# Optimization experiments

Hardware: AMD Instinct MI355X
Metric: run time of the kernel (lower is better)

Reference implementation:

```python
import jax, jax.numpy as jnp
import numpy as np

B, T, D, E = 8, 2048, 256, 4
D_E = D // E


def setup_inputs() -> dict:
    key = jax.random.key(0)
    ks = jax.random.split(key, 12)
    s = 1.0 / np.sqrt(D)
    x = jax.random.normal(ks[0], (B, T, D), dtype=jnp.float32)
    # ensure max(seq_len) == T so the padded input matches this_batch_padlen
    seq_len = jnp.concatenate([
        jax.random.randint(ks[1], (B - 1,), T // 2, T),
        jnp.array([T]),
    ]).astype(jnp.int32)
    return {
        "x": x,
        "seq_len": seq_len,
        "wq": jax.random.uniform(ks[2], (D, D), jnp.float32, -s, s),
        "bq": jax.random.uniform(ks[3], (D,), jnp.float32, -s, s),
        "wk": jax.random.uniform(ks[4], (D, D), jnp.float32, -s, s),
        "bk": jax.random.uniform(ks[5], (D,), jnp.float32, -s, s),
        "wv": jax.random.uniform(ks[6], (D, D), jnp.float32, -s, s),
        "bv": jax.random.uniform(ks[7], (D,), jnp.float32, -s, s),
        "wo": jax.random.uniform(ks[8], (D, D), jnp.float32, -s, s),
        "bo": jax.random.uniform(ks[9], (D,), jnp.float32, -s, s),
        "theta": jnp.array([50.0], dtype=jnp.float32),
    }


def _split_heads(y):
    # faithful to torch: [B,T,D] -> permute(0,2,1) -> [B,D,T] -> reshape(B*E, T, D_E)
    return jnp.transpose(y, (0, 2, 1)).reshape(B * E, T, D_E)


def reference(x, seq_len, wq, bq, wk, bk, wv, bv, wo, bo, theta):
    Q = _split_heads(x @ wq.T + bq)          # [B*E, T, D_E]
    K = _split_heads(x @ wk.T + bk)          # [B*E, T, D_E]
    V = _split_heads(x @ wv.T + bv)          # [B*E, T, D_E]

    # padding mask: zero out query rows (and key cols) past seq_len[i]
    pos = jnp.arange(T)
    valid = (pos[None, :] < seq_len[:, None])                 # [B, T]
    mask_q = jnp.repeat(valid, E, axis=0).astype(Q.dtype)     # [B*E, T]
    Q = Q * mask_q[:, :, None]
    K = K * mask_q[:, :, None]

    scale = jnp.sqrt(jnp.float32(T))
    att = jnp.einsum('bqd,bkd->bqk', Q, K) / scale            # [B*E, T, T]

    # Gaussian positional penalty (is_punish=True)
    tpos = jnp.arange(T, dtype=jnp.float32)
    diff = tpos[None, :] - tpos[:, None]                      # j - i
    punish = jnp.exp(-(diff ** 2) / (theta[0] ** 2))          # [T, T]
    att = att * punish[None, :, :]

    att = jnp.where(att == 0.0, jnp.float32(-2e20), att)
    att = jax.nn.softmax(att, axis=2)

    ctx = jnp.einsum('bqk,bkd->bqd', att, V)                  # [B*E, T, D_E]
    # faithful inverse of _split_heads: permute(0,2,1)->reshape(B,D,T)->permute
    ctx = jnp.transpose(jnp.transpose(ctx, (0, 2, 1)).reshape(B, D, T), (0, 2, 1))
    A = ctx @ wo.T + bo
    return A + x
```

## Files before the change

### kernel.cpp

```cpp
#include <hip/hip_runtime.h>
#include <hip/hip_bf16.h>
#include <math.h>
#include <stdint.h>

#define B_SZ   8
#define T_SEQ  2048
#define DIM    256
#define NH     32
#define DE     64
#define BAND   509
#define M_ROWS (B_SZ * T_SEQ)

typedef __attribute__((ext_vector_type(8))) short short8;
typedef __attribute__((ext_vector_type(4))) float floatx4;
typedef __attribute__((ext_vector_type(4))) unsigned uintx4;
typedef unsigned short ushort_t;

__device__ __forceinline__ ushort_t f2bf(float x) {
    unsigned u = __float_as_uint(x);
    u += 0x7fffu + ((u >> 16) & 1u);
    return (ushort_t)(u >> 16);
}
__device__ __forceinline__ float bf2f(ushort_t b) {
    return __uint_as_float(((unsigned)b) << 16);
}
__device__ __forceinline__ unsigned pack2(float a, float b) {
    unsigned lo = __bfloat16_as_ushort(__float2bfloat16(a));
    unsigned hi = __bfloat16_as_ushort(__float2bfloat16(b));
    return lo | (hi << 16);
}

__device__ __forceinline__ double pd_exact(int d, float th) {
    float df  = (float)d;
    float arg = (-(df * df)) / (th * th);
    double pdd = exp((double)arg);
    if (pdd < 1.17549435082228751e-38)
        return rint(pdd * 0x1p149) * 0x1p-149;
    return (double)(float)pdd;
}

__global__ __launch_bounds__(256) void prep_kernel(
    const float* __restrict__ x,
    const float* __restrict__ wq, const float* __restrict__ wk,
    const float* __restrict__ wv, const float* __restrict__ wo,
    const float* __restrict__ theta,
    ushort_t* __restrict__ xb, ushort_t* __restrict__ wb,
    float* __restrict__ thr_g, float* __restrict__ pdf_g)
{
    const int bid = blockIdx.x, tid = threadIdx.x;
    if (bid < 2048) {
        size_t i8 = ((size_t)bid * 256 + tid) * 8;
        float4 a = *(const float4*)(x + i8);
        float4 b = *(const float4*)(x + i8 + 4);
        uint4 o;
        o.x = pack2(a.x, a.y); o.y = pack2(a.z, a.w);
        o.z = pack2(b.x, b.y); o.w = pack2(b.z, b.w);
        *(uint4*)(xb + i8) = o;
    } else if (bid < 2176) {
        size_t w8 = ((size_t)(bid - 2048) * 256 + tid) * 8;
        int which = (int)(w8 >> 16);
        const float* src = (which == 0) ? wq : (which == 1) ? wk : (which == 2) ? wv : wo;
        size_t off = w8 & 65535;
        float4 a = *(const float4*)(src + off);
        float4 b = *(const float4*)(src + off + 4);
        uint4 o;
        o.x = pack2(a.x, a.y); o.y = pack2(a.z, a.w);
        o.z = pack2(b.x, b.y); o.w = pack2(b.z, b.w);
        *(uint4*)(wb + w8) = o;
    } else {
        int i = (bid - 2176) * 256 + tid;
        float th = theta[0];
        if (i < 1024) {
            int d = i - 512;
            pdf_g[i] = (float)pd_exact(d, th) * 1.44269504088896340736f;
        }
        if (i < 1536) {
            int d = i - 768;
            int ad = d < 0 ? -d : d;
            if (ad < 321) {
                thr_g[i] = __builtin_inff();
            } else {
                double pdv = pd_exact(ad, th);
                thr_g[i] = (pdv == 0.0) ? __builtin_inff() : (float)(0x1p-150 / pdv);
            }
        }
    }
}

__global__ __launch_bounds__(256, 2) void proj_qkv_mfma(
    const ushort_t* __restrict__ xb, const ushort_t* __restrict__ wb,
    const float* __restrict__ bq, const float* __restrict__ bk,
    const float* __restrict__ bv, const int* __restrict__ seq_len,
    ushort_t* __restrict__ Qh, ushort_t* __restrict__ Kh, ushort_t* __restrict__ Vh)
{
    __shared__ __align__(16) ushort_t As[64][264];
    __shared__ __align__(16) ushort_t Ls[4][64][68];
    const int tid = threadIdx.x;
    const int wave = tid >> 6, lane = tid & 63;
    const int quad = lane >> 4, l15 = lane & 15;
    const int task = blockIdx.x * 4 + wave;
    const int nt64 = task % 12;
    const int mstrip = task / 12;
    const int mode = nt64 >> 2;
    const int nloc_base = (nt64 & 3) * 64;
    const ushort_t* Wp = wb + (size_t)mode * 65536;
    const int m0 = mstrip * 64;
    const int bb = m0 >> 11;
    const int th0 = (m0 >> 6) & 31;
    const int sl = seq_len[bb];
    ushort_t* outp = (mode == 0) ? Qh : (mode == 1) ? Kh : Vh;
    const float* bias = (mode == 0) ? bq : (mode == 1) ? bk : bv;
    const int hh = bb * 4 + (nloc_base >> 6);
    const float oscale = (mode == 0) ? 0.022097086912079612f : 1.0f;

    #pragma unroll
    for (int rep = 0; rep < 8; ++rep) {
        int f = rep * 256 + tid;
        int row = f >> 5, c8 = (f & 31) * 8;
        *(uint4*)&As[row][c8] = *(const uint4*)(xb + (size_t)(m0 + row) * 256 + c8);
    }

    short8 Bf[4][8];
    #pragma unroll
    for (int nt = 0; nt < 4; ++nt) {
        int nrow = nloc_base + nt * 16 + l15;
        #pragma unroll
        for (int ks = 0; ks < 8; ++ks)
            Bf[nt][ks] = *(const short8*)(Wp + (size_t)nrow * 256 + ks * 32 + quad * 8);
    }
    float bias4[4];
    #pragma unroll
    for (int nt = 0; nt < 4; ++nt) bias4[nt] = bias[nloc_base + nt * 16 + l15];

    __syncthreads();

    #pragma unroll
    for (int mb = 0; mb < 4; ++mb) {
        short8 Af[8];
        #pragma unroll
        for (int ks = 0; ks < 8; ++ks)
            Af[ks] = *(const short8*)&As[mb * 16 + l15][ks * 32 + quad * 8];
        floatx4 acc[4];
        #pragma unroll
        for (int nt = 0; nt < 4; ++nt) acc[nt] = (floatx4){0.f, 0.f, 0.f, 0.f};
        #pragma unroll
        for (int ks = 0; ks < 8; ++ks)
            #pragma unroll
            for (int nt = 0; nt < 4; ++nt)
                acc[nt] = __builtin_amdgcn_mfma_f32_16x16x32_bf16(Af[ks], Bf[nt][ks], acc[nt], 0, 0, 0);
        #pragma unroll
        for (int nt = 0; nt < 4; ++nt) {
            float v0 = (acc[nt][0] + bias4[nt]) * oscale;
            float v1 = (acc[nt][1] + bias4[nt]) * oscale;
            float v2 = (acc[nt][2] + bias4[nt]) * oscale;
            float v3 = (acc[nt][3] + bias4[nt]) * oscale;
            uint2 pk; pk.x = pack2(v0, v1); pk.y = pack2(v2, v3);
            *(uint2*)&Ls[wave][nt * 16 + l15][mb * 16 + quad * 4] = pk;
        }
    }

    #pragma unroll
    for (int s = 0; s < 16; ++s) {
        int dl = s * 4 + quad;
        int e0 = l15 * 4;
        uint2 pk = *(const uint2*)&Ls[wave][dl][e0];
        int q = dl * 32 + th0;
        if (mode <= 1 && q >= sl) { pk.x = 0u; pk.y = 0u; }
        *(uint2*)(outp + (((size_t)hh * T_SEQ + q) << 6) + e0) = pk;
    }
}

__global__ __launch_bounds__(256) void vtrans_kernel(const ushort_t* __restrict__ Vh,
                                                     ushort_t* __restrict__ VTp,
                                                     float* __restrict__ mv)
{
    __shared__ ushort_t Vs[256][66];
    __shared__ float red[32][72];
    const int tid = threadIdx.x;
    const int h = blockIdx.x >> 3, chunk = blockIdx.x & 7;
    const ushort_t* src = Vh + ((size_t)(h * T_SEQ + chunk * 256)) * DE;
    float s[8] = {};
    #pragma unroll
    for (int rep = 0; rep < 8; ++rep) {
        int f = rep * 256 + tid;
        int row = f >> 3, c8 = (f & 7) * 8;
        uint4 u = *(const uint4*)(src + (size_t)row * DE + c8);
        *(uint4*)&Vs[row][c8] = u;
        const ushort_t* w = (const ushort_t*)&u;
        #pragma unroll
        for (int i = 0; i < 8; ++i) s[i] += bf2f(w[i]);
    }
    {
        const int r0 = tid >> 3, es = (tid & 7) * 8;
        #pragma unroll
        for (int i = 0; i < 8; ++i) red[r0][es + i] = s[i];
    }
    __syncthreads();
    if (tid < 64) {
        float t = 0.f;
        #pragma unroll
        for (int g = 0; g < 32; ++g) t += red[g][tid];
        atomicAdd(&mv[h * DE + tid], t);
    }
    const int w = tid >> 6, lane = tid & 63;
    const int half = lane >> 5;
    const int c32 = lane & 31;
    const int cbase = c32 * 8;
    const int blk = cbase >> 6;
    const int cin = cbase & 63;
    #pragma unroll
    for (int rr = 0; rr < 8; ++rr) {
        int e = w * 16 + rr * 2 + half;
        ushort_t tmp[8];
        #pragma unroll
        for (int t = 0; t < 8; ++t) {
            int ci = cin + t;
            int j = blk * 64 + 32 * (ci >> 5) + 4 * ((ci >> 3) & 3)
                  + 16 * ((ci >> 2) & 1) + (ci & 3);
            tmp[t] = Vs[j][e];
        }
        *(uint4*)(VTp + ((size_t)(h * DE + e)) * T_SEQ + chunk * 256 + cbase) = *(uint4*)tmp;
    }
}

__global__ __launch_bounds__(512) void attn_mfma_kernel(
    const ushort_t* __restrict__ Qh, const ushort_t* __restrict__ Kh,
    const ushort_t* __restrict__ VTp, const float* __restrict__ thr_g,
    const float* __restrict__ pdf_g, const float* __restrict__ mvs,
    const int* __restrict__ seq_len, ushort_t* __restrict__ ctxb)
{
    __shared__ ushort_t Ks [2][64][72];
    __shared__ ushort_t VTs[2][64][72];
    __shared__ float pdfl[1024];
    __shared__ float thrc[1536];

    const int tid  = threadIdx.x;
    const int wave = tid >> 6;
    const int lane = tid & 63;
    const int quad = lane >> 4;
    const int l15  = lane & 15;
    const int bid   = blockIdx.x;
    const int inner = bid >> 3;
    const int g     = inner >> 4;
    const int strip = ((inner & 15) + g * 4) & 15;
    const int h  = (g << 3) | (bid & 7);
    const int q0 = strip * 128;
    const int b  = h >> 2;
    const int sl = seq_len[b];
    const float invT = 1.0f / (float)T_SEQ;
    ushort_t* outbase = ctxb + ((size_t)b * T_SEQ + q0) * DIM + (size_t)(h & 3) * 64;

    if (q0 >= sl) {
        #pragma unroll
        for (int nt = 0; nt < 4; ++nt) {
            ushort_t mval = f2bf(mvs[h * DE + l15 + 16 * nt] * invT);
            #pragma unroll
            for (int r = 0; r < 4; ++r)
                outbase[(size_t)(wave * 16 + quad * 4 + r) * DIM + l15 + 16 * nt] = mval;
        }
        return;
    }

    for (int i = tid; i < 1024; i += 512) pdfl[i] = pdf_g[i];
    for (int i = tid; i < 1536; i += 512) thrc[i] = thr_g[i];

    short8 qa0, qa1;
    {
        const ushort_t* qp = Qh + ((size_t)h * T_SEQ + q0 + wave * 16 + l15) * DE + quad * 8;
        qa0 = *(const short8*)(qp);
        qa1 = *(const short8*)(qp + 32);
    }

    float l_acc = 0.f;
    floatx4 cacc[4];
    #pragma unroll
    for (int nt = 0; nt < 4; ++nt) cacc[nt] = (floatx4){0.f, 0.f, 0.f, 0.f};

    int jlo = q0 - BAND;       if (jlo < 0) jlo = 0;
    int jhi = q0 + 127 + BAND; if (jhi > sl - 1) jhi = sl - 1;
    const int jt0 = jlo >> 6, jt1 = jhi >> 6;

    const int krow = tid >> 3;
    const int kc8  = (tid & 7) * 8;
    const ushort_t* Kbp = Kh + (size_t)h * T_SEQ * DE;
    const ushort_t* Vbp = VTp + (size_t)h * DE * T_SEQ;
    uint4 kpre0, kpre1, vpre0, vpre1;
    {
        const int ja = jt0 << 6;
        const int jb = ((jt0 + 1 <= jt1) ? jt0 + 1 : jt1) << 6;
        kpre0 = *(const uint4*)(Kbp + (size_t)(ja + krow) * DE + kc8);
        vpre0 = *(const uint4*)(Vbp + (size_t)krow * T_SEQ + ja + kc8);
        kpre1 = *(const uint4*)(Kbp + (size_t)(jb + krow) * DE + kc8);
        vpre1 = *(const uint4*)(Vbp + (size_t)krow * T_SEQ + jb + kc8);
    }

    const int qrow = q0 + wave * 16 + l15;

    auto subtile = [&](int s, int j0s) {
        floatx4 ST[4];
        #pragma unroll
        for (int nt = 0; nt < 4; ++nt) {
            short8 ka0 = *(const short8*)&Ks[s][l15 + 16 * nt][quad * 8];
            short8 ka1 = *(const short8*)&Ks[s][l15 + 16 * nt][32 + quad * 8];
            floatx4 z = {0.f, 0.f, 0.f, 0.f};
            z = __builtin_amdgcn_mfma_f32_16x16x32_bf16(ka0, qa0, z, 0, 0, 0);
            z = __builtin_amdgcn_mfma_f32_16x16x32_bf16(ka1, qa1, z, 0, 0, 0);
            ST[nt] = z;
        }

        const int offw = j0s - q0 - wave * 16;
        const int db   = j0s + quad * 4 - qrow;
        float p[4][4];
        if (offw > -384 && offw < 336) {
            if (j0s + 63 < sl) {
                #pragma unroll
                for (int nt = 0; nt < 4; ++nt)
                    #pragma unroll
                    for (int r = 0; r < 4; ++r)
                        p[nt][r] = __builtin_amdgcn_exp2f(
                            ST[nt][r] * pdfl[db + 512 + nt * 16 + r]);
            } else {
                #pragma unroll
                for (int nt = 0; nt < 4; ++nt)
                    #pragma unroll
                    for (int r = 0; r < 4; ++r) {
                        float v = __builtin_amdgcn_exp2f(
                            ST[nt][r] * pdfl[db + 512 + nt * 16 + r]);
                        p[nt][r] = (j0s + nt * 16 + quad * 4 + r < sl) ? v : 0.f;
                    }
            }
        } else {
            #pragma unroll
            for (int nt = 0; nt < 4; ++nt)
                #pragma unroll
                for (int r = 0; r < 4; ++r)
                    p[nt][r] = (fabsf(ST[nt][r]) > thrc[db + 768 + nt * 16 + r])
                               ? 1.0f : 0.0f;
        }

        #pragma unroll
        for (int nt = 0; nt < 4; ++nt)
            l_acc += (p[nt][0] + p[nt][1]) + (p[nt][2] + p[nt][3]);

        uintx4 t0, t1;
        t0.x = pack2(p[0][0], p[0][1]); t0.y = pack2(p[0][2], p[0][3]);
        t0.z = pack2(p[1][0], p[1][1]); t0.w = pack2(p[1][2], p[1][3]);
        t1.x = pack2(p[2][0], p[2][1]); t1.y = pack2(p[2][2], p[2][3]);
        t1.z = pack2(p[3][0], p[3][1]); t1.w = pack2(p[3][2], p[3][3]);
        short8 pa0 = __builtin_bit_cast(short8, t0);
        short8 pa1 = __builtin_bit_cast(short8, t1);

        #pragma unroll
        for (int nt = 0; nt < 4; ++nt) {
            short8 vb0 = *(const short8*)&VTs[s][l15 + 16 * nt][quad * 8];
            short8 vb1 = *(const short8*)&VTs[s][l15 + 16 * nt][32 + quad * 8];
            floatx4 c = cacc[nt];
            c = __builtin_amdgcn_mfma_f32_16x16x32_bf16(pa0, vb0, c, 0, 0, 0);
            c = __builtin_amdgcn_mfma_f32_16x16x32_bf16(pa1, vb1, c, 0, 0, 0);
            cacc[nt] = c;
        }
    };

    for (int jt = jt0; jt <= jt1; jt += 2) {
        const int j0a = jt << 6;
        const bool has_b = (jt + 1 <= jt1);
        const int j0b = (has_b ? jt + 1 : jt1) << 6;
        __syncthreads();
        *(uint4*)&Ks [0][krow][kc8] = kpre0;
        *(uint4*)&VTs[0][krow][kc8] = vpre0;
        *(uint4*)&Ks [1][krow][kc8] = kpre1;
        *(uint4*)&VTs[1][krow][kc8] = vpre1;
        __syncthreads();
        if (jt + 2 <= jt1) {
            const int jn0 = (jt + 2) << 6;
            const int jn1 = ((jt + 3 <= jt1) ? jt + 3 : jt1) << 6;
            kpre0 = *(const uint4*)(Kbp + (size_t)(jn0 + krow) * DE + kc8);
            vpre0 = *(const uint4*)(Vbp + (size_t)krow * T_SEQ + jn0 + kc8);
            kpre1 = *(const uint4*)(Kbp + (size_t)(jn1 + krow) * DE + kc8);
            vpre1 = *(const uint4*)(Vbp + (size_t)krow * T_SEQ + jn1 + kc8);
        }
        subtile(0, j0a);
        if (has_b) subtile(1, j0b);
    }

    l_acc += __shfl_xor(l_acc, 16);
    l_acc += __shfl_xor(l_acc, 32);
    const float linv = 1.0f / l_acc;
    float linv4[4];
    #pragma unroll
    for (int r = 0; r < 4; ++r) linv4[r] = __shfl(linv, quad * 4 + r);

    #pragma unroll
    for (int nt = 0; nt < 4; ++nt) {
        #pragma unroll
        for (int r = 0; r < 4; ++r) {
            int row = wave * 16 + quad * 4 + r;
            int qg = q0 + row;
            float o = cacc[nt][r] * linv4[r];
            if (qg >= sl) o = mvs[h * DE + l15 + 16 * nt] * invT;
            outbase[(size_t)row * DIM + l15 + 16 * nt] = f2bf(o);
        }
    }
}

__global__ __launch_bounds__(256, 2) void proj_o_mfma(
    const ushort_t* __restrict__ ctx, const ushort_t* __restrict__ wb,
    const float* __restrict__ bo, const float* __restrict__ x,
    float* __restrict__ out)
{
    __shared__ __align__(16) ushort_t As[32][264];
    const int tid = threadIdx.x;
    const int wave = tid >> 6, lane = tid & 63;
    const int quad = lane >> 4, l15 = lane & 15;
    const int m0 = blockIdx.x * 32;
    const int n0 = wave * 64;
    const ushort_t* Wp = wb + (size_t)3 * 65536;

    #pragma unroll
    for (int rep = 0; rep < 4; ++rep) {
        int f = rep * 256 + tid;
        int row = f >> 5, c8 = (f & 31) * 8;
        *(uint4*)&As[row][c8] = *(const uint4*)(ctx + (size_t)(m0 + row) * 256 + c8);
    }

    short8 Bf[4][8];
    #pragma unroll
    for (int nt = 0; nt < 4; ++nt) {
        int nrow = n0 + nt * 16 + l15;
        #pragma unroll
        for (int ks = 0; ks < 8; ++ks)
            Bf[nt][ks] = *(const short8*)(Wp + (size_t)nrow * 256 + ks * 32 + quad * 8);
    }
    float bias4[4];
    #pragma unroll
    for (int nt = 0; nt < 4; ++nt) bias4[nt] = bo[n0 + nt * 16 + l15];

    __syncthreads();

    #pragma unroll
    for (int mb = 0; mb < 2; ++mb) {
        short8 Af[8];
        #pragma unroll
        for (int ks = 0; ks < 8; ++ks)
            Af[ks] = *(const short8*)&As[mb * 16 + l15][ks * 32 + quad * 8];
        floatx4 acc[4];
        #pragma unroll
        for (int nt = 0; nt < 4; ++nt) acc[nt] = (floatx4){0.f, 0.f, 0.f, 0.f};
        #pragma unroll
        for (int ks = 0; ks < 8; ++ks)
            #pragma unroll
            for (int nt = 0; nt < 4; ++nt)
                acc[nt] = __builtin_amdgcn_mfma_f32_16x16x32_bf16(Af[ks], Bf[nt][ks], acc[nt], 0, 0, 0);
        #pragma unroll
        for (int nt = 0; nt < 4; ++nt) {
            int d = n0 + nt * 16 + l15;
            #pragma unroll
            for (int r = 0; r < 4; ++r) {
                size_t mi = (size_t)(m0 + mb * 16 + quad * 4 + r) * 256 + d;
                out[mi] = acc[nt][r] + bias4[nt] + x[mi];
            }
        }
    }
}

extern "C" void kernel_launch(void* const* d_in, const int* in_sizes, int n_in,
                              void* d_out, int out_size, void* d_ws, size_t ws_size,
                              hipStream_t stream)
{
    (void)in_sizes; (void)n_in; (void)out_size; (void)ws_size;
    const float* x  = (const float*)d_in[0];
    const int*   sl = (const int*)d_in[1];
    const float* wq = (const float*)d_in[2];
    const float* bq = (const float*)d_in[3];
    const float* wk = (const float*)d_in[4];
    const float* bk = (const float*)d_in[5];
    const float* wv = (const float*)d_in[6];
    const float* bv = (const float*)d_in[7];
    const float* wo = (const float*)d_in[8];
    const float* bo = (const float*)d_in[9];
    const float* th = (const float*)d_in[10];
    float* out = (float*)d_out;

    char* ws = (char*)d_ws;
    const size_t SZH = (size_t)M_ROWS * DIM * sizeof(ushort_t);
    ushort_t* xb  = (ushort_t*)(ws);
    ushort_t* wb  = (ushort_t*)(ws + SZH);
    ushort_t* Qh  = (ushort_t*)(ws + SZH + 524288);
    ushort_t* Kh  = (ushort_t*)(ws + 2*SZH + 524288);
    ushort_t* Vh  = (ushort_t*)(ws + 3*SZH + 524288);
    ushort_t* VTp = (ushort_t*)(ws + 4*SZH + 524288);
    ushort_t* Cb  = (ushort_t*)(ws + 5*SZH + 524288);
    float*    Mv  = (float*)   (ws + 6*SZH + 524288);
    float*    Thr = (float*)   (ws + 6*SZH + 524288 + 8192);
    float*    Pdf = (float*)   (ws + 6*SZH + 524288 + 8192 + 6144);

    hipMemsetAsync(Mv, 0, NH * DE * sizeof(float), stream);
    prep_kernel<<<dim3(2186), dim3(256), 0, stream>>>(x, wq, wk, wv, wo, th, xb, wb, Thr, Pdf);
    proj_qkv_mfma<<<dim3(768), dim3(256), 0, stream>>>(xb, wb, bq, bk, bv, sl, Qh, Kh, Vh);
    vtrans_kernel<<<dim3(NH * 8), dim3(256), 0, stream>>>(Vh, VTp, Mv);
    attn_mfma_kernel<<<dim3(512), dim3(512), 0, stream>>>(Qh, Kh, VTp, Thr, Pdf, Mv, sl, Cb);
    proj_o_mfma<<<dim3(512), dim3(256), 0, stream>>>(Cb, wb, bo, x, out);
}
```

Measured before the change: 158.0 us.

## Fuse x bf16 conversion into QKV projection with one block per row strip

The separate prep pass that converted x to bf16 is removed. The QKV projection now loads fp32 x directly and packs it to bf16 in shared memory. Each block now has 12 waves (768 threads), one per 64-column output tile of Q/K/V, so an x row strip is staged once and shared by all three projections instead of being reloaded by three blocks. This removes a full bf16 write and read of x, at the cost of more shared memory (12 Ls tiles), one block per CU, and fewer blocks (256).

```diff
diff --git a/kernel.cpp b/kernel.cpp
--- a/kernel.cpp
+++ b/kernel.cpp
@@ -40,24 +40,15 @@
 }
 
 __global__ __launch_bounds__(256) void prep_kernel(
-    const float* __restrict__ x,
     const float* __restrict__ wq, const float* __restrict__ wk,
     const float* __restrict__ wv, const float* __restrict__ wo,
     const float* __restrict__ theta,
-    ushort_t* __restrict__ xb, ushort_t* __restrict__ wb,
+    ushort_t* __restrict__ wb,
     float* __restrict__ thr_g, float* __restrict__ pdf_g)
 {
     const int bid = blockIdx.x, tid = threadIdx.x;
-    if (bid < 2048) {
-        size_t i8 = ((size_t)bid * 256 + tid) * 8;
-        float4 a = *(const float4*)(x + i8);
-        float4 b = *(const float4*)(x + i8 + 4);
-        uint4 o;
-        o.x = pack2(a.x, a.y); o.y = pack2(a.z, a.w);
-        o.z = pack2(b.x, b.y); o.w = pack2(b.z, b.w);
-        *(uint4*)(xb + i8) = o;
-    } else if (bid < 2176) {
-        size_t w8 = ((size_t)(bid - 2048) * 256 + tid) * 8;
+    if (bid < 128) {
+        size_t w8 = ((size_t)bid * 256 + tid) * 8;
         int which = (int)(w8 >> 16);
         const float* src = (which == 0) ? wq : (which == 1) ? wk : (which == 2) ? wv : wo;
         size_t off = w8 & 65535;
@@ -68,7 +59,7 @@
         o.z = pack2(b.x, b.y); o.w = pack2(b.z, b.w);
         *(uint4*)(wb + w8) = o;
     } else {
-        int i = (bid - 2176) * 256 + tid;
+        int i = (bid - 128) * 256 + tid;
         float th = theta[0];
         if (i < 1024) {
             int d = i - 512;
@@ -87,20 +78,19 @@
     }
 }
 
-__global__ __launch_bounds__(256, 2) void proj_qkv_mfma(
-    const ushort_t* __restrict__ xb, const ushort_t* __restrict__ wb,
+__global__ __launch_bounds__(768, 1) void proj_qkv_mfma(
+    const float* __restrict__ x, const ushort_t* __restrict__ wb,
     const float* __restrict__ bq, const float* __restrict__ bk,
     const float* __restrict__ bv, const int* __restrict__ seq_len,
     ushort_t* __restrict__ Qh, ushort_t* __restrict__ Kh, ushort_t* __restrict__ Vh)
 {
     __shared__ __align__(16) ushort_t As[64][264];
-    __shared__ __align__(16) ushort_t Ls[4][64][68];
+    __shared__ __align__(16) ushort_t Ls[12][64][68];
     const int tid = threadIdx.x;
     const int wave = tid >> 6, lane = tid & 63;
     const int quad = lane >> 4, l15 = lane & 15;
-    const int task = blockIdx.x * 4 + wave;
-    const int nt64 = task % 12;
-    const int mstrip = task / 12;
+    const int mstrip = blockIdx.x;
+    const int nt64 = wave;
     const int mode = nt64 >> 2;
     const int nloc_base = (nt64 & 3) * 64;
     const ushort_t* Wp = wb + (size_t)mode * 65536;
@@ -113,11 +103,15 @@
     const int hh = bb * 4 + (nloc_base >> 6);
     const float oscale = (mode == 0) ? 0.022097086912079612f : 1.0f;
 
-    #pragma unroll
-    for (int rep = 0; rep < 8; ++rep) {
-        int f = rep * 256 + tid;
+    for (int f = tid; f < 2048; f += 768) {
         int row = f >> 5, c8 = (f & 31) * 8;
-        *(uint4*)&As[row][c8] = *(const uint4*)(xb + (size_t)(m0 + row) * 256 + c8);
+        const float* sp = x + (size_t)(m0 + row) * 256 + c8;
+        float4 a = *(const float4*)(sp);
+        float4 b = *(const float4*)(sp + 4);
+        uint4 o;
+        o.x = pack2(a.x, a.y); o.y = pack2(a.z, a.w);
+        o.z = pack2(b.x, b.y); o.w = pack2(b.z, b.w);
+        *(uint4*)&As[row][c8] = o;
     }
 
     short8 Bf[4][8];
@@ -483,20 +477,19 @@
 
     char* ws = (char*)d_ws;
     const size_t SZH = (size_t)M_ROWS * DIM * sizeof(ushort_t);
-    ushort_t* xb  = (ushort_t*)(ws);
-    ushort_t* wb  = (ushort_t*)(ws + SZH);
-    ushort_t* Qh  = (ushort_t*)(ws + SZH + 524288);
-    ushort_t* Kh  = (ushort_t*)(ws + 2*SZH + 524288);
-    ushort_t* Vh  = (ushort_t*)(ws + 3*SZH + 524288);
-    ushort_t* VTp = (ushort_t*)(ws + 4*SZH + 524288);
-    ushort_t* Cb  = (ushort_t*)(ws + 5*SZH + 524288);
-    float*    Mv  = (float*)   (ws + 6*SZH + 524288);
-    float*    Thr = (float*)   (ws + 6*SZH + 524288 + 8192);
-    float*    Pdf = (float*)   (ws + 6*SZH + 524288 + 8192 + 6144);
+    ushort_t* wb  = (ushort_t*)(ws);
+    ushort_t* Qh  = (ushort_t*)(ws + 524288);
+    ushort_t* Kh  = (ushort_t*)(ws + SZH + 524288);
+    ushort_t* Vh  = (ushort_t*)(ws + 2*SZH + 524288);
+    ushort_t* VTp = (ushort_t*)(ws + 3*SZH + 524288);
+    ushort_t* Cb  = (ushort_t*)(ws + 4*SZH + 524288);
+    float*    Mv  = (float*)   (ws + 5*SZH + 524288);
+    float*    Thr = (float*)   (ws + 5*SZH + 524288 + 8192);
+    float*    Pdf = (float*)   (ws + 5*SZH + 524288 + 8192 + 6144);
 
     hipMemsetAsync(Mv, 0, NH * DE * sizeof(float), stream);
-    prep_kernel<<<dim3(2186), dim3(256), 0, stream>>>(x, wq, wk, wv, wo, th, xb, wb, Thr, Pdf);
-    proj_qkv_mfma<<<dim3(768), dim3(256), 0, stream>>>(xb, wb, bq, bk, bv, sl, Qh, Kh, Vh);
+    prep_kernel<<<dim3(138), dim3(256), 0, stream>>>(wq, wk, wv, wo, th, wb, Thr, Pdf);
+    proj_qkv_mfma<<<dim3(256), dim3(768), 0, stream>>>(x, wb, bq, bk, bv, sl, Qh, Kh, Vh);
     vtrans_kernel<<<dim3(NH * 8), dim3(256), 0, stream>>>(Vh, VTp, Mv);
     attn_mfma_kernel<<<dim3(512), dim3(512), 0, stream>>>(Qh, Kh, VTp, Thr, Pdf, Mv, sl, Cb);
     proj_o_mfma<<<dim3(512), dim3(256), 0, stream>>>(Cb, wb, bo, x, out);
```

Measured after the change: 176.2 us. 11.5% more time.
